# Kernel optimization log

Measured on AMD Instinct MI355X. Metric: run time of the kernel, lower is better.

The kernel has to match this reference:

```python
import jax, jax.numpy as jnp
import numpy as np

N, E, D, H = 16000, 256000, 128, 4
ALPHA = 0.2  # LeakyReLU negative slope


def setup_inputs() -> dict:
    key = jax.random.key(0)
    ks = jax.random.split(key, 9)
    s = 0.1
    return {
        "h": jax.random.normal(ks[0], (N, D), jnp.float32),
        "W": jax.random.normal(ks[1], (H, D, D), jnp.float32) * s,
        "a": jax.random.normal(ks[2], (H, 2 * D), jnp.float32) * s,
        "W_ih": jax.random.normal(ks[3], (3 * D, H * D), jnp.float32) * s,
        "W_hh": jax.random.normal(ks[4], (3 * D, D), jnp.float32) * s,
        "b_ih": jnp.zeros((3 * D,), jnp.float32),
        "b_hh": jnp.zeros((3 * D,), jnp.float32),
        "src": jax.random.randint(ks[5], (E,), 0, N, jnp.int32),
        "dst": jax.random.randint(ks[6], (E,), 0, N, jnp.int32),
    }


def reference(h, W, a, W_ih, W_hh, b_ih, b_hh, src, dst):
    n = h.shape[0]
    # Per-head linear transform: Wh[n,h,d]
    Wh = jnp.einsum("nd,hde->nhe", h, W)
    a1, a2 = a[:, :D], a[:, D:]
    s_src = jnp.einsum("nhd,hd->nh", Wh, a1)  # src attention logits
    s_dst = jnp.einsum("nhd,hd->nh", Wh, a2)  # dst attention logits
    e = jax.nn.leaky_relu(s_src[src] + s_dst[dst], ALPHA)  # [E,H]
    # Segment softmax over incoming edges of each dst node
    m = jax.ops.segment_max(e, dst, num_segments=n)          # [N,H]
    ex = jnp.exp(e - m[dst])
    denom = jax.ops.segment_sum(ex, dst, num_segments=n)     # [N,H]
    att = ex / denom[dst]                                    # [E,H]
    # Weighted message aggregation: h_prime[n,h,d]
    h_prime = jax.ops.segment_sum(att[:, :, None] * Wh[src], dst, num_segments=n)
    x = h_prime.reshape(n, H * D)  # concat heads
    # PyTorch GRUCell(input=H*D, hidden=D)
    gi = x @ W_ih.T + b_ih
    gh = h @ W_hh.T + b_hh
    i_r, i_z, i_n = jnp.split(gi, 3, axis=1)
    h_r, h_z, h_n = jnp.split(gh, 3, axis=1)
    r = jax.nn.sigmoid(i_r + h_r)
    z = jax.nn.sigmoid(i_z + h_z)
    nvec = jnp.tanh(i_n + r * h_n)
    return (1.0 - z) * nvec + z * h
```

## Files before the change

### kernel.cpp

```cpp
#include <hip/hip_runtime.h>
#include <math.h>

#define N_NODES 16000
#define E_EDGES 256000
#define DIM 128
#define HEADS 4
#define LRELU_ALPHA 0.2f
#define SLOT 64

typedef unsigned short u16;
typedef unsigned int u32;
typedef short bf16x8 __attribute__((ext_vector_type(8)));
typedef float floatx4 __attribute__((ext_vector_type(4)));

#define AS1 __attribute__((address_space(1)))
#define AS3 __attribute__((address_space(3)))

__device__ __forceinline__ u16 f2bf(float f) {
    u32 u = __float_as_uint(f);
    u32 r = (u + 0x7fffu + ((u >> 16) & 1u)) >> 16;
    return (u16)r;
}
__device__ __forceinline__ float bflo(u32 v) { return __uint_as_float(v << 16); }
__device__ __forceinline__ float bfhi(u32 v) { return __uint_as_float(v & 0xffff0000u); }
__device__ __forceinline__ float bfs(u16 v) { return __uint_as_float((u32)v << 16); }
__device__ __forceinline__ u32 pack2(float lo, float hi) {
    return (u32)f2bf(lo) | ((u32)f2bf(hi) << 16);
}


__global__ __launch_bounds__(256) void prep_kernel(
    const float* __restrict__ W, const float* __restrict__ a,
    const float* __restrict__ W_ih, const float* __restrict__ W_hh,
    const int* __restrict__ src, const int* __restrict__ dst,
    u16* __restrict__ Wihb, u16* __restrict__ Wb,
    u16* __restrict__ Wcat, float* __restrict__ wa1, float* __restrict__ wa2,
    u32* __restrict__ cnt, int* __restrict__ ssort)
{
    const int b = blockIdx.x;
    const int tid = threadIdx.x;
    if (b < 1000) {
        int e = b * 256 + tid;
        u32 base = cnt[N_NODES];
        int d = dst[e];
        u32 pos = atomicAdd(&cnt[d], 1u) - base;
        ssort[d * SLOT + pos] = src[e];
    } else if (b < 1768) {
        int i = (b - 1000) * 256 + tid;
        Wihb[i] = f2bf(W_ih[i]);
        if (i < HEADS * DIM * DIM) Wb[i] = f2bf(W[i]);
    } else if (b < 1960) {
        int t = (b - 1768) * 256 + tid;
        int jp = t >> 7, e = t & 127;
        int gate = jp >> 7;
        if (gate == 2) gate = 3;
        int p = (jp & 127) * 4 + gate;
        Wcat[(size_t)p * 640 + 512 + e] = f2bf(W_hh[jp * 128 + e]);
    } else if (b < 2280) {
        int t = (b - 1960) * 256 + tid;
        if (t < 16384) {
            int d = t >> 7, e = t & 127;
            Wcat[(size_t)(d * 4 + 2) * 640 + 512 + e] = 0;
        } else {
            int t2 = t - 16384;
            int d = t2 >> 9, c = t2 & 511;
            Wcat[(size_t)(d * 4 + 3) * 640 + c] = 0;
        }
    } else {
        int t = (b - 2280) * 256 + tid;
        int h = t >> 7;
        const float* wrow = W + (long)t * DIM;
        const float* a1 = a + h * 2 * DIM;
        const float* a2 = a1 + DIM;
        float s1 = 0.f, s2 = 0.f;
        for (int e = 0; e < DIM; ++e) {
            float w = wrow[e];
            s1 = fmaf(w, a1[e], s1);
            s2 = fmaf(w, a2[e], s2);
        }
        wa1[t] = s1;
        wa2[t] = s2;
    }
}

__device__ __forceinline__ void score_wave(int n, const float* __restrict__ hin,
    const float* __restrict__ wa1, const float* __restrict__ wa2,
    float* __restrict__ s_src, float* __restrict__ s_dst, u16* __restrict__ xcat, int lane)
{
    float2 hv = ((const float2*)hin)[n * 64 + lane];
    ((u32*)xcat)[n * 320 + 256 + lane] = pack2(hv.x, hv.y);
    float ps[4], qs[4];
    #pragma unroll
    for (int h = 0; h < 4; ++h) {
        float2 w1 = ((const float2*)(wa1 + h * 128))[lane];
        float2 w2 = ((const float2*)(wa2 + h * 128))[lane];
        float p = hv.x * w1.x + hv.y * w1.y;
        float q = hv.x * w2.x + hv.y * w2.y;
        #pragma unroll
        for (int off = 32; off > 0; off >>= 1) {
            p += __shfl_xor(p, off, 64);
            q += __shfl_xor(q, off, 64);
        }
        ps[h] = p; qs[h] = q;
    }
    if (lane == 0) {
        #pragma unroll
        for (int h = 0; h < 4; ++h) {
            s_src[n * HEADS + h] = ps[h];
            s_dst[n * HEADS + h] = qs[h];
        }
    }
}

template<int PERM_C>
__device__ __forceinline__ void gemm_tile(const u16* A, const u16* Bt, u16* C,
    int kstart, int kend, int lda, int ldb, int ldc, int row0, int col0, char* SMp, int tid)
{
    u16 (*Alds)[32] = (u16(*)[32])SMp;
    u16 (*Blds)[32] = (u16(*)[32])(SMp + 8192);
    const int wave = tid >> 6;
    const int lane = tid & 63;
    const int quad = lane >> 4;
    const int l15  = lane & 15;
    const int wm = (wave >> 1) * 64;
    const int wn = (wave & 1) * 64;
    const int ch0 = wave * 2;
    const int srow = lane >> 2;
    const int scol = (lane & 3) * 8;

    floatx4 acc[4][4] = {};

    for (int k0 = kstart; k0 < kend; k0 += 32) {
        #pragma unroll
        for (int c = 0; c < 2; ++c) {
            int ch = ch0 + c;
            const u16* ga = A + (size_t)(row0 + ch * 16 + srow) * lda + k0 + scol;
            __builtin_amdgcn_global_load_lds((AS1 void*)ga, (AS3 void*)&Alds[ch * 16][0], 16, 0, 0);
            const u16* gb = Bt + (size_t)(col0 + ch * 16 + srow) * ldb + k0 + scol;
            __builtin_amdgcn_global_load_lds((AS1 void*)gb, (AS3 void*)&Blds[ch * 16][0], 16, 0, 0);
        }
        __syncthreads();
        bf16x8 af[4], bfr[4];
        #pragma unroll
        for (int i = 0; i < 4; ++i) af[i] = *(const bf16x8*)&Alds[wm + i * 16 + l15][quad * 8];
        #pragma unroll
        for (int j = 0; j < 4; ++j) bfr[j] = *(const bf16x8*)&Blds[wn + j * 16 + l15][quad * 8];
        #pragma unroll
        for (int i = 0; i < 4; ++i)
            #pragma unroll
            for (int j = 0; j < 4; ++j)
                acc[i][j] = __builtin_amdgcn_mfma_f32_16x16x32_bf16(af[i], bfr[j], acc[i][j], 0, 0, 0);
        __syncthreads();
    }
    #pragma unroll
    for (int i = 0; i < 4; ++i) {
        #pragma unroll
        for (int r = 0; r < 4; ++r) {
            int row = row0 + wm + i * 16 + quad * 4 + r;
            if (PERM_C) row = (row & 127) * 4 + (row >> 7);
            size_t base = (size_t)row * ldc + col0 + wn + l15;
            #pragma unroll
            for (int j = 0; j < 4; ++j) C[base + j * 16] = f2bf(acc[i][j][r]);
        }
    }
}

__global__ __launch_bounds__(256) void mt_scores_kernel(
    const u16* __restrict__ Wihb, const u16* __restrict__ Wb, u16* __restrict__ Wcat,
    const float* __restrict__ hin, const float* __restrict__ wa1, const float* __restrict__ wa2,
    float* __restrict__ s_src, float* __restrict__ s_dst, u16* __restrict__ xcat)
{
    __shared__ __align__(16) char SM[16384];
    const int tid = threadIdx.x;
    const int b = blockIdx.x;
    if (b < 12) {
        int y = b % 3, z = b / 3;
        gemm_tile<1>(Wihb + z * 128, Wb + (size_t)z * 16384, Wcat + z * 128,
                     0, 128, 512, 128, 640, y * 128, 0, SM, tid);
    } else {
        for (int n = (b - 12) * 4 + (tid >> 6); n < N_NODES; n += 1024 * 4)
            score_wave(n, hin, wa1, wa2, s_src, s_dst, xcat, tid & 63);
    }
}

__global__ __launch_bounds__(256) void aggregate_kernel(
    const float* __restrict__ s_src, const float* __restrict__ s_dst,
    const u32* __restrict__ cnt, const int* __restrict__ srcs,
    u16* __restrict__ xcat)
{
    const int tid = threadIdx.x;
    const int lane = tid & 63;
    const int n = blockIdx.x * 4 + (tid >> 6);
    const u32 base = cnt[N_NODES];
    const int deg = (int)(cnt[n] - base);
    const int start = n * SLOT;
    u32* xrow = (u32*)(xcat + (size_t)n * 640);
    if (deg == 0) {
        #pragma unroll
        for (int h = 0; h < 4; ++h) xrow[h * 64 + lane] = 0u;
        return;
    }
    const u32* hb = (const u32*)xcat;
    const float sd = s_dst[n * HEADS + (lane & 3)];
    const int j16 = lane >> 2;
    const int hh  = lane & 3;

    float2 acc[4] = {{0.f,0.f},{0.f,0.f},{0.f,0.f},{0.f,0.f}};
    float dsum[4] = {0.f, 0.f, 0.f, 0.f};

    for (int cb = 0; cb < deg; cb += 16) {
        const int clen = min(16, deg - cb);
        int sv = 0;
        if (lane < clen) sv = srcs[start + cb + lane];
        float wv = 0.f;
        if (j16 < clen) {
            int s = __shfl(sv, j16, 64);
            float e = s_src[s * HEADS + hh] + sd;
            e = e > 0.f ? e : LRELU_ALPHA * e;
            wv = __expf(e);
        }
        int e = 0;
        for (; e + 8 <= clen; e += 8) {
            u32 vs[8];
            #pragma unroll
            for (int k = 0; k < 8; ++k) {
                int s = __shfl(sv, e + k, 64);
                vs[k] = hb[s * 320 + 256 + lane];
            }
            #pragma unroll
            for (int k = 0; k < 8; ++k) {
                float lo = bflo(vs[k]), hi = bfhi(vs[k]);
                #pragma unroll
                for (int h = 0; h < 4; ++h) {
                    float w = __shfl(wv, (e + k) * 4 + h, 64);
                    acc[h].x = fmaf(w, lo, acc[h].x);
                    acc[h].y = fmaf(w, hi, acc[h].y);
                    dsum[h] += w;
                }
            }
        }
        for (; e < clen; ++e) {
            int s = __shfl(sv, e, 64);
            u32 v = hb[s * 320 + 256 + lane];
            float lo = bflo(v), hi = bfhi(v);
            #pragma unroll
            for (int h = 0; h < 4; ++h) {
                float w = __shfl(wv, e * 4 + h, 64);
                acc[h].x = fmaf(w, lo, acc[h].x);
                acc[h].y = fmaf(w, hi, acc[h].y);
                dsum[h] += w;
            }
        }
    }
    #pragma unroll
    for (int h = 0; h < 4; ++h) {
        float invd = 1.f / dsum[h];
        xrow[h * 64 + lane] = pack2(acc[h].x * invd, acc[h].y * invd);
    }
}

__global__ __launch_bounds__(256) void gemm_gru_kernel(
    const u16* __restrict__ xcat, const u16* __restrict__ Wcat,
    const float* __restrict__ b_ih, const float* __restrict__ b_hh,
    const float* __restrict__ hin, float* __restrict__ out)
{
    __shared__ __align__(16) char SM[32768];
    u16 (*Alds)[32] = (u16(*)[32])SM;
    u16 (*Blds)[32] = (u16(*)[32])(SM + 8192);
    u16 (*tile)[128] = (u16(*)[128])SM;
    const int tid = threadIdx.x;
    const int wave = tid >> 6;
    const int lane = tid & 63;
    const int quad = lane >> 4;
    const int l15  = lane & 15;
    const int row0 = blockIdx.y * 128;
    const int col0 = blockIdx.x * 128;
    const int wm = (wave >> 1) * 64;
    const int wn = (wave & 1) * 64;
    const int ch0 = wave * 2;
    const int srow = lane >> 2;
    const int scol = (lane & 3) * 8;

    floatx4 acc[4][4] = {};

    for (int k0 = 0; k0 < 640; k0 += 32) {
        #pragma unroll
        for (int c = 0; c < 2; ++c) {
            int ch = ch0 + c;
            const u16* ga = xcat + (size_t)(row0 + ch * 16 + srow) * 640 + k0 + scol;
            __builtin_amdgcn_global_load_lds((AS1 void*)ga, (AS3 void*)&Alds[ch * 16][0], 16, 0, 0);
            const u16* gb = Wcat + (size_t)(col0 + ch * 16 + srow) * 640 + k0 + scol;
            __builtin_amdgcn_global_load_lds((AS1 void*)gb, (AS3 void*)&Blds[ch * 16][0], 16, 0, 0);
        }
        __syncthreads();
        bf16x8 af[4], bfr[4];
        #pragma unroll
        for (int i = 0; i < 4; ++i) af[i] = *(const bf16x8*)&Alds[wm + i * 16 + l15][quad * 8];
        #pragma unroll
        for (int j = 0; j < 4; ++j) bfr[j] = *(const bf16x8*)&Blds[wn + j * 16 + l15][quad * 8];
        #pragma unroll
        for (int i = 0; i < 4; ++i)
            #pragma unroll
            for (int j = 0; j < 4; ++j)
                acc[i][j] = __builtin_amdgcn_mfma_f32_16x16x32_bf16(af[i], bfr[j], acc[i][j], 0, 0, 0);
        __syncthreads();
    }
    #pragma unroll
    for (int i = 0; i < 4; ++i)
        #pragma unroll
        for (int r = 0; r < 4; ++r) {
            int row = wm + i * 16 + quad * 4 + r;
            #pragma unroll
            for (int j = 0; j < 4; ++j)
                tile[row][wn + j * 16 + l15] = f2bf(acc[i][j][r]);
        }
    __syncthreads();
    const int dim_l = tid & 31;
    const int rg = tid >> 5;
    const int dim_g = col0 / 4 + dim_l;
    const float bir = b_ih[dim_g],       bhr = b_hh[dim_g];
    const float biz = b_ih[128 + dim_g], bhz = b_hh[128 + dim_g];
    const float bin = b_ih[256 + dim_g], bhn = b_hh[256 + dim_g];
    #pragma unroll
    for (int i = 0; i < 16; ++i) {
        int row = rg * 16 + i;
        int node = row0 + row;
        ushort4 gv = *(const ushort4*)&tile[row][dim_l * 4];
        float A  = bfs(gv.x) + bir + bhr;
        float B  = bfs(gv.y) + biz + bhz;
        float Cn = bfs(gv.z) + bin;
        float Dn = bfs(gv.w) + bhn;
        float r = 1.f / (1.f + __expf(-A));
        float z = 1.f / (1.f + __expf(-B));
        float e2 = __expf(2.f * (Cn + r * Dn));
        float nv = (e2 - 1.f) / (e2 + 1.f);
        out[(size_t)node * 128 + dim_g] = (1.f - z) * nv + z * hin[(size_t)node * 128 + dim_g];
    }
}

extern "C" void kernel_launch(void* const* d_in, const int* in_sizes, int n_in,
                              void* d_out, int out_size, void* d_ws, size_t ws_size,
                              hipStream_t stream)
{
    const float* h    = (const float*)d_in[0];
    const float* W    = (const float*)d_in[1];
    const float* a    = (const float*)d_in[2];
    const float* W_ih = (const float*)d_in[3];
    const float* W_hh = (const float*)d_in[4];
    const float* b_ih = (const float*)d_in[5];
    const float* b_hh = (const float*)d_in[6];
    const int*   src  = (const int*)d_in[7];
    const int*   dst  = (const int*)d_in[8];
    float* out = (float*)d_out;

    char* ws = (char*)d_ws;
    size_t off = 0;
    auto alloc = [&](size_t bytes) { void* p = ws + off; off += (bytes + 255) & ~(size_t)255; return p; };

    u16*   xcat = (u16*)alloc((size_t)N_NODES * 640 * 2);
    u16*   Wihb = (u16*)alloc(384 * 512 * 2);
    u16*   Wb   = (u16*)alloc(HEADS * DIM * DIM * 2);
    u16*   Wcat = (u16*)alloc(512 * 640 * 2);
    float* wa1  = (float*)alloc(512 * 4);
    float* wa2  = (float*)alloc(512 * 4);
    float* s_src = (float*)alloc((size_t)N_NODES * HEADS * 4);
    float* s_dst = (float*)alloc((size_t)N_NODES * HEADS * 4);
    u32*   cnt  = (u32*)alloc((N_NODES + 1) * 4);
    int*   ssort = (int*)alloc((size_t)N_NODES * SLOT * 4);

    prep_kernel<<<2282, 256, 0, stream>>>(
        W, a, W_ih, W_hh, src, dst, Wihb, Wb, Wcat, wa1, wa2, cnt, ssort);

    mt_scores_kernel<<<1036, 256, 0, stream>>>(
        Wihb, Wb, Wcat, h, wa1, wa2, s_src, s_dst, xcat);

    aggregate_kernel<<<N_NODES / 4, 256, 0, stream>>>(s_src, s_dst, cnt, ssort, xcat);

    gemm_gru_kernel<<<dim3(4, 125), 256, 0, stream>>>(xcat, Wcat, b_ih, b_hh, h, out);
}
```

Baseline: 145.4 us.

## Fuse weight-product GEMM into prep kernel and double K-step in GRU GEMM

The W_ih·W weight-product tiles are now computed inside the prep kernel straight from fp32 inputs, converting to bf16 while staging into LDS. This removes the separate bf16 copies of W_ih and W and their global round trip. The score computation becomes its own kernel with a simpler grid. The final GEMM+GRU kernel now loads 64 K-columns per barrier pair instead of 32, halving its synchronization count at the cost of doubled LDS staging. The prep kernel now carries 16KB of shared memory in every block, which may lower occupancy for the edge-sorting blocks.

```diff
diff --git a/kernel.cpp b/kernel.cpp
--- a/kernel.cpp
+++ b/kernel.cpp
@@ -29,14 +29,65 @@
 }
 
 
+__device__ __forceinline__ void mt_tile(const float* __restrict__ W_ih,
+    const float* __restrict__ W, u16* __restrict__ Wcat, int y, int z, char* SMp, int tid)
+{
+    u16 (*Alds)[32] = (u16(*)[32])SMp;
+    u16 (*Blds)[32] = (u16(*)[32])(SMp + 8192);
+    const int wave = tid >> 6;
+    const int lane = tid & 63;
+    const int quad = lane >> 4;
+    const int l15  = lane & 15;
+    const int wm = (wave >> 1) * 64;
+    const int wn = (wave & 1) * 64;
+    const int jrow = tid >> 1;
+    const int eh = (tid & 1) * 16;
+
+    floatx4 acc[4][4] = {};
+
+    for (int k0 = 0; k0 < 128; k0 += 32) {
+        const float* arow = W_ih + (size_t)(y * 128 + jrow) * 512 + z * 128 + k0 + eh;
+        const float* brow = W + (size_t)(z * 128 + jrow) * 128 + k0 + eh;
+        #pragma unroll
+        for (int i = 0; i < 16; ++i) {
+            Alds[jrow][eh + i] = f2bf(arow[i]);
+            Blds[jrow][eh + i] = f2bf(brow[i]);
+        }
+        __syncthreads();
+        bf16x8 af[4], bfr[4];
+        #pragma unroll
+        for (int i = 0; i < 4; ++i) af[i] = *(const bf16x8*)&Alds[wm + i * 16 + l15][quad * 8];
+        #pragma unroll
+        for (int j = 0; j < 4; ++j) bfr[j] = *(const bf16x8*)&Blds[wn + j * 16 + l15][quad * 8];
+        #pragma unroll
+        for (int i = 0; i < 4; ++i)
+            #pragma unroll
+            for (int j = 0; j < 4; ++j)
+                acc[i][j] = __builtin_amdgcn_mfma_f32_16x16x32_bf16(af[i], bfr[j], acc[i][j], 0, 0, 0);
+        __syncthreads();
+    }
+    u16* C = Wcat + z * 128;
+    #pragma unroll
+    for (int i = 0; i < 4; ++i) {
+        #pragma unroll
+        for (int r = 0; r < 4; ++r) {
+            int row = y * 128 + wm + i * 16 + quad * 4 + r;
+            int p = (row & 127) * 4 + (row >> 7);
+            size_t base = (size_t)p * 640 + wn + l15;
+            #pragma unroll
+            for (int j = 0; j < 4; ++j) C[base + j * 16] = f2bf(acc[i][j][r]);
+        }
+    }
+}
+
 __global__ __launch_bounds__(256) void prep_kernel(
     const float* __restrict__ W, const float* __restrict__ a,
     const float* __restrict__ W_ih, const float* __restrict__ W_hh,
     const int* __restrict__ src, const int* __restrict__ dst,
-    u16* __restrict__ Wihb, u16* __restrict__ Wb,
     u16* __restrict__ Wcat, float* __restrict__ wa1, float* __restrict__ wa2,
     u32* __restrict__ cnt, int* __restrict__ ssort)
 {
+    __shared__ __align__(16) char SM[16384];
     const int b = blockIdx.x;
     const int tid = threadIdx.x;
     if (b < 1000) {
@@ -45,19 +96,15 @@
         int d = dst[e];
         u32 pos = atomicAdd(&cnt[d], 1u) - base;
         ssort[d * SLOT + pos] = src[e];
-    } else if (b < 1768) {
-        int i = (b - 1000) * 256 + tid;
-        Wihb[i] = f2bf(W_ih[i]);
-        if (i < HEADS * DIM * DIM) Wb[i] = f2bf(W[i]);
-    } else if (b < 1960) {
-        int t = (b - 1768) * 256 + tid;
+    } else if (b < 1192) {
+        int t = (b - 1000) * 256 + tid;
         int jp = t >> 7, e = t & 127;
         int gate = jp >> 7;
         if (gate == 2) gate = 3;
         int p = (jp & 127) * 4 + gate;
         Wcat[(size_t)p * 640 + 512 + e] = f2bf(W_hh[jp * 128 + e]);
-    } else if (b < 2280) {
-        int t = (b - 1960) * 256 + tid;
+    } else if (b < 1512) {
+        int t = (b - 1192) * 256 + tid;
         if (t < 16384) {
             int d = t >> 7, e = t & 127;
             Wcat[(size_t)(d * 4 + 2) * 640 + 512 + e] = 0;
@@ -66,8 +113,8 @@
             int d = t2 >> 9, c = t2 & 511;
             Wcat[(size_t)(d * 4 + 3) * 640 + c] = 0;
         }
-    } else {
-        int t = (b - 2280) * 256 + tid;
+    } else if (b < 1514) {
+        int t = (b - 1512) * 256 + tid;
         int h = t >> 7;
         const float* wrow = W + (long)t * DIM;
         const float* a1 = a + h * 2 * DIM;
@@ -80,106 +127,43 @@
         }
         wa1[t] = s1;
         wa2[t] = s2;
-    }
-}
-
-__device__ __forceinline__ void score_wave(int n, const float* __restrict__ hin,
-    const float* __restrict__ wa1, const float* __restrict__ wa2,
-    float* __restrict__ s_src, float* __restrict__ s_dst, u16* __restrict__ xcat, int lane)
-{
-    float2 hv = ((const float2*)hin)[n * 64 + lane];
-    ((u32*)xcat)[n * 320 + 256 + lane] = pack2(hv.x, hv.y);
-    float ps[4], qs[4];
-    #pragma unroll
-    for (int h = 0; h < 4; ++h) {
-        float2 w1 = ((const float2*)(wa1 + h * 128))[lane];
-        float2 w2 = ((const float2*)(wa2 + h * 128))[lane];
-        float p = hv.x * w1.x + hv.y * w1.y;
-        float q = hv.x * w2.x + hv.y * w2.y;
-        #pragma unroll
-        for (int off = 32; off > 0; off >>= 1) {
-            p += __shfl_xor(p, off, 64);
-            q += __shfl_xor(q, off, 64);
-        }
-        ps[h] = p; qs[h] = q;
-    }
-    if (lane == 0) {
-        #pragma unroll
-        for (int h = 0; h < 4; ++h) {
-            s_src[n * HEADS + h] = ps[h];
-            s_dst[n * HEADS + h] = qs[h];
-        }
-    }
-}
-
-template<int PERM_C>
-__device__ __forceinline__ void gemm_tile(const u16* A, const u16* Bt, u16* C,
-    int kstart, int kend, int lda, int ldb, int ldc, int row0, int col0, char* SMp, int tid)
-{
-    u16 (*Alds)[32] = (u16(*)[32])SMp;
-    u16 (*Blds)[32] = (u16(*)[32])(SMp + 8192);
-    const int wave = tid >> 6;
-    const int lane = tid & 63;
-    const int quad = lane >> 4;
-    const int l15  = lane & 15;
-    const int wm = (wave >> 1) * 64;
-    const int wn = (wave & 1) * 64;
-    const int ch0 = wave * 2;
-    const int srow = lane >> 2;
-    const int scol = (lane & 3) * 8;
-
-    floatx4 acc[4][4] = {};
-
-    for (int k0 = kstart; k0 < kend; k0 += 32) {
-        #pragma unroll
-        for (int c = 0; c < 2; ++c) {
-            int ch = ch0 + c;
-            const u16* ga = A + (size_t)(row0 + ch * 16 + srow) * lda + k0 + scol;
-            __builtin_amdgcn_global_load_lds((AS1 void*)ga, (AS3 void*)&Alds[ch * 16][0], 16, 0, 0);
-            const u16* gb = Bt + (size_t)(col0 + ch * 16 + srow) * ldb + k0 + scol;
-            __builtin_amdgcn_global_load_lds((AS1 void*)gb, (AS3 void*)&Blds[ch * 16][0], 16, 0, 0);
-        }
-        __syncthreads();
-        bf16x8 af[4], bfr[4];
-        #pragma unroll
-        for (int i = 0; i < 4; ++i) af[i] = *(const bf16x8*)&Alds[wm + i * 16 + l15][quad * 8];
-        #pragma unroll
-        for (int j = 0; j < 4; ++j) bfr[j] = *(const bf16x8*)&Blds[wn + j * 16 + l15][quad * 8];
-        #pragma unroll
-        for (int i = 0; i < 4; ++i)
-            #pragma unroll
-            for (int j = 0; j < 4; ++j)
-                acc[i][j] = __builtin_amdgcn_mfma_f32_16x16x32_bf16(af[i], bfr[j], acc[i][j], 0, 0, 0);
-        __syncthreads();
-    }
-    #pragma unroll
-    for (int i = 0; i < 4; ++i) {
-        #pragma unroll
-        for (int r = 0; r < 4; ++r) {
-            int row = row0 + wm + i * 16 + quad * 4 + r;
-            if (PERM_C) row = (row & 127) * 4 + (row >> 7);
-            size_t base = (size_t)row * ldc + col0 + wn + l15;
-            #pragma unroll
-            for (int j = 0; j < 4; ++j) C[base + j * 16] = f2bf(acc[i][j][r]);
-        }
-    }
-}
-
-__global__ __launch_bounds__(256) void mt_scores_kernel(
-    const u16* __restrict__ Wihb, const u16* __restrict__ Wb, u16* __restrict__ Wcat,
+    } else {
+        int t = b - 1514;
+        mt_tile(W_ih, W, Wcat, t % 3, t / 3, SM, tid);
+    }
+}
+
+__global__ __launch_bounds__(256) void scores_kernel(
     const float* __restrict__ hin, const float* __restrict__ wa1, const float* __restrict__ wa2,
     float* __restrict__ s_src, float* __restrict__ s_dst, u16* __restrict__ xcat)
 {
-    __shared__ __align__(16) char SM[16384];
     const int tid = threadIdx.x;
-    const int b = blockIdx.x;
-    if (b < 12) {
-        int y = b % 3, z = b / 3;
-        gemm_tile<1>(Wihb + z * 128, Wb + (size_t)z * 16384, Wcat + z * 128,
-                     0, 128, 512, 128, 640, y * 128, 0, SM, tid);
-    } else {
-        for (int n = (b - 12) * 4 + (tid >> 6); n < N_NODES; n += 1024 * 4)
-            score_wave(n, hin, wa1, wa2, s_src, s_dst, xcat, tid & 63);
+    const int lane = tid & 63;
+    const int n = blockIdx.x * 4 + (tid >> 6);
+    for (int nn = n; nn < N_NODES; nn += 4000) {
+        float2 hv = ((const float2*)hin)[nn * 64 + lane];
+        ((u32*)xcat)[nn * 320 + 256 + lane] = pack2(hv.x, hv.y);
+        float ps[4], qs[4];
+        #pragma unroll
+        for (int h = 0; h < 4; ++h) {
+            float2 w1 = ((const float2*)(wa1 + h * 128))[lane];
+            float2 w2 = ((const float2*)(wa2 + h * 128))[lane];
+            float p = hv.x * w1.x + hv.y * w1.y;
+            float q = hv.x * w2.x + hv.y * w2.y;
+            #pragma unroll
+            for (int off = 32; off > 0; off >>= 1) {
+                p += __shfl_xor(p, off, 64);
+                q += __shfl_xor(q, off, 64);
+            }
+            ps[h] = p; qs[h] = q;
+        }
+        if (lane == 0) {
+            #pragma unroll
+            for (int h = 0; h < 4; ++h) {
+                s_src[nn * HEADS + h] = ps[h];
+                s_dst[nn * HEADS + h] = qs[h];
+            }
+        }
     }
 }
 
@@ -266,7 +250,7 @@
 {
     __shared__ __align__(16) char SM[32768];
     u16 (*Alds)[32] = (u16(*)[32])SM;
-    u16 (*Blds)[32] = (u16(*)[32])(SM + 8192);
+    u16 (*Blds)[32] = (u16(*)[32])(SM + 16384);
     u16 (*tile)[128] = (u16(*)[128])SM;
     const int tid = threadIdx.x;
     const int wave = tid >> 6;
@@ -283,26 +267,32 @@
 
     floatx4 acc[4][4] = {};
 
-    for (int k0 = 0; k0 < 640; k0 += 32) {
-        #pragma unroll
-        for (int c = 0; c < 2; ++c) {
-            int ch = ch0 + c;
-            const u16* ga = xcat + (size_t)(row0 + ch * 16 + srow) * 640 + k0 + scol;
-            __builtin_amdgcn_global_load_lds((AS1 void*)ga, (AS3 void*)&Alds[ch * 16][0], 16, 0, 0);
-            const u16* gb = Wcat + (size_t)(col0 + ch * 16 + srow) * 640 + k0 + scol;
-            __builtin_amdgcn_global_load_lds((AS1 void*)gb, (AS3 void*)&Blds[ch * 16][0], 16, 0, 0);
+    for (int k0 = 0; k0 < 640; k0 += 64) {
+        #pragma unroll
+        for (int kh = 0; kh < 2; ++kh) {
+            #pragma unroll
+            for (int c = 0; c < 2; ++c) {
+                int ch = ch0 + c;
+                const u16* ga = xcat + (size_t)(row0 + ch * 16 + srow) * 640 + k0 + kh * 32 + scol;
+                __builtin_amdgcn_global_load_lds((AS1 void*)ga, (AS3 void*)&Alds[kh * 128 + ch * 16][0], 16, 0, 0);
+                const u16* gb = Wcat + (size_t)(col0 + ch * 16 + srow) * 640 + k0 + kh * 32 + scol;
+                __builtin_amdgcn_global_load_lds((AS1 void*)gb, (AS3 void*)&Blds[kh * 128 + ch * 16][0], 16, 0, 0);
+            }
         }
         __syncthreads();
-        bf16x8 af[4], bfr[4];
-        #pragma unroll
-        for (int i = 0; i < 4; ++i) af[i] = *(const bf16x8*)&Alds[wm + i * 16 + l15][quad * 8];
-        #pragma unroll
-        for (int j = 0; j < 4; ++j) bfr[j] = *(const bf16x8*)&Blds[wn + j * 16 + l15][quad * 8];
-        #pragma unroll
-        for (int i = 0; i < 4; ++i)
-            #pragma unroll
-            for (int j = 0; j < 4; ++j)
-                acc[i][j] = __builtin_amdgcn_mfma_f32_16x16x32_bf16(af[i], bfr[j], acc[i][j], 0, 0, 0);
+        #pragma unroll
+        for (int kh = 0; kh < 2; ++kh) {
+            bf16x8 af[4], bfr[4];
+            #pragma unroll
+            for (int i = 0; i < 4; ++i) af[i] = *(const bf16x8*)&Alds[kh * 128 + wm + i * 16 + l15][quad * 8];
+            #pragma unroll
+            for (int j = 0; j < 4; ++j) bfr[j] = *(const bf16x8*)&Blds[kh * 128 + wn + j * 16 + l15][quad * 8];
+            #pragma unroll
+            for (int i = 0; i < 4; ++i)
+                #pragma unroll
+                for (int j = 0; j < 4; ++j)
+                    acc[i][j] = __builtin_amdgcn_mfma_f32_16x16x32_bf16(af[i], bfr[j], acc[i][j], 0, 0, 0);
+        }
         __syncthreads();
     }
     #pragma unroll
@@ -358,8 +348,6 @@
     auto alloc = [&](size_t bytes) { void* p = ws + off; off += (bytes + 255) & ~(size_t)255; return p; };
 
     u16*   xcat = (u16*)alloc((size_t)N_NODES * 640 * 2);
-    u16*   Wihb = (u16*)alloc(384 * 512 * 2);
-    u16*   Wb   = (u16*)alloc(HEADS * DIM * DIM * 2);
     u16*   Wcat = (u16*)alloc(512 * 640 * 2);
     float* wa1  = (float*)alloc(512 * 4);
     float* wa2  = (float*)alloc(512 * 4);
@@ -368,11 +356,10 @@
     u32*   cnt  = (u32*)alloc((N_NODES + 1) * 4);
     int*   ssort = (int*)alloc((size_t)N_NODES * SLOT * 4);
 
-    prep_kernel<<<2282, 256, 0, stream>>>(
-        W, a, W_ih, W_hh, src, dst, Wihb, Wb, Wcat, wa1, wa2, cnt, ssort);
-
-    mt_scores_kernel<<<1036, 256, 0, stream>>>(
-        Wihb, Wb, Wcat, h, wa1, wa2, s_src, s_dst, xcat);
+    prep_kernel<<<1526, 256, 0, stream>>>(
+        W, a, W_ih, W_hh, src, dst, Wcat, wa1, wa2, cnt, ssort);
+
+    scores_kernel<<<1000, 256, 0, stream>>>(h, wa1, wa2, s_src, s_dst, xcat);
 
     aggregate_kernel<<<N_NODES / 4, 256, 0, stream>>>(s_src, s_dst, cnt, ssort, xcat);
 
```

Result: faster. 142.2 us (median of 2 runs) (-2.2%).
